# Kernel optimization log

Hardware: AMD Instinct MI355X
Metric: run time of the kernel (lower is better)

Reference implementation:

```python
import jax, jax.numpy as jnp
import numpy as np


def _gcn_conv(x, edge_index, edge_weight, W, b, n_nodes):
    # PyG GCNConv with normalize=True: add self-loops (weight 1), symmetric norm,
    # transform then aggregate: out[col] += norm * (x @ W)[row], plus bias.
    row = jnp.concatenate([edge_index[0], jnp.arange(n_nodes)])
    col = jnp.concatenate([edge_index[1], jnp.arange(n_nodes)])
    w = jnp.concatenate([edge_weight, jnp.ones((n_nodes,), x.dtype)])
    deg = jax.ops.segment_sum(w, col, num_segments=n_nodes)
    dinv = jnp.where(deg > 0, jax.lax.rsqrt(jnp.maximum(deg, 1e-12)), 0.0)
    norm = dinv[row] * w * dinv[col]            # [E+N]
    h = x @ W                                   # [N, out]
    msg = h[row] * norm[:, None]                # [E+N, out]
    out = jax.ops.segment_sum(msg, col, num_segments=n_nodes)
    return out + b


def setup_inputs() -> dict:
    key = jax.random.key(0)
    ks = jax.random.split(key, 6)
    N, E, F_IN, H, C = 50000, 800000, 512, 128, 40
    features = jax.random.normal(ks[0], (N, F_IN), jnp.float32)
    edge_index = jax.random.randint(ks[1], (2, E), 0, N, jnp.int64)
    edge_weight = jax.random.uniform(ks[2], (E,), jnp.float32)
    W1 = jax.random.normal(ks[3], (F_IN, H), jnp.float32) * 0.05
    b1 = jnp.zeros((H,), jnp.float32)
    W2 = jax.random.normal(ks[4], (H, C), jnp.float32) * 0.05
    b2 = jnp.zeros((C,), jnp.float32)
    return {"features": features, "edge_index": edge_index, "edge_weight": edge_weight,
            "W1": W1, "b1": b1, "W2": W2, "b2": b2}


def reference(features, edge_index, edge_weight, W1, b1, W2, b2):
    n_nodes = features.shape[0]
    x = _gcn_conv(features, edge_index, edge_weight, W1, b1, n_nodes)
    x = jax.nn.relu(x)
    # F.dropout(training=self.training): identity in eval mode
    x = _gcn_conv(x, edge_index, edge_weight, W2, b2, n_nodes)
    return jax.nn.log_softmax(x, axis=1)
```

## Files before the change

kernel.cpp:

```cpp
#include <hip/hip_runtime.h>
#include <math.h>

#define FIN  512
#define HDIM 128
#define CDIM 40
#define CPAD 48
#define H2P  40
#define CAP  64

typedef __attribute__((ext_vector_type(8))) short shortx8;
typedef __attribute__((ext_vector_type(4))) float f32x4;

__device__ inline unsigned short f2bf(float x) {
    unsigned u = __builtin_bit_cast(unsigned, x);
    unsigned r = u + 0x7fffu + ((u >> 16) & 1u);
    return (unsigned short)(r >> 16);
}
__device__ inline float bfu(unsigned short v) { return __builtin_bit_cast(float, (unsigned)v << 16); }
__device__ inline float bflo(unsigned u) { return __builtin_bit_cast(float, u << 16); }
__device__ inline float bfhi(unsigned u) { return __builtin_bit_cast(float, u & 0xffff0000u); }
__device__ inline float wdec(unsigned p) { return __builtin_bit_cast(float, (p & 0x7fffu) << 16); }

__global__ void k_fill(const int* __restrict__ row, const int* __restrict__ col,
                       const float* __restrict__ w,
                       unsigned long long* __restrict__ cursor,
                       unsigned* __restrict__ bkt, int E) {
    int e = blockIdx.x * blockDim.x + threadIdx.x;
    if (e >= E) return;
    const int c = col[e];
    const float we = w[e];
    const unsigned long long wfix = (unsigned long long)(we * 4294967296.0f);
    const unsigned long long old = atomicAdd(&cursor[c], (1ULL << 40) | wfix);
    const int p = (int)(old >> 40);
    const unsigned wb = (__builtin_bit_cast(unsigned, we) + 0x8000u) >> 16;
    if (p < CAP) bkt[(size_t)c * CAP + p] = ((unsigned)row[e] << 15) | (wb & 0x7fffu);
}

#define PREPB 280
__global__ void k_prep(const float* __restrict__ W1, const float* __restrict__ W2,
                       unsigned short* __restrict__ W1T, unsigned short* __restrict__ W2T,
                       const unsigned long long* __restrict__ cursor,
                       int* __restrict__ cnt, float* __restrict__ dinv, int n) {
    const int b = blockIdx.x;
    if (b < PREPB) {
        const int i = b * 256 + threadIdx.x;
        if (i < FIN * HDIM) {
            const int k = i >> 7, nn = i & 127;
            W1T[nn * FIN + k] = f2bf(W1[i]);
        } else {
            const int j = i - FIN * HDIM;
            const int nn = j >> 7, k = j & 127;
            W2T[j] = (nn < CDIM) ? f2bf(W2[k * CDIM + nn]) : (unsigned short)0;
        }
    } else {
        const int i = (b - PREPB) * 256 + threadIdx.x;
        if (i < n) {
            const unsigned long long p = cursor[i];
            cnt[i] = min((int)(p >> 40), CAP);
            const float wsum = (float)(p & ((1ULL << 40) - 1)) * 2.3283064365386963e-10f;
            dinv[i] = rsqrtf(1.0f + wsum);
        }
    }
}

#define G1_LDA 72
__global__ __launch_bounds__(256) void k_gemm1(const float* __restrict__ A,
                                               const unsigned short* __restrict__ W1T,
                                               const float* __restrict__ dinv,
                                               unsigned short* __restrict__ h1bf, int M) {
    __shared__ short As[128 * G1_LDA];
    __shared__ short Bs[128 * G1_LDA];
    const int tid  = threadIdx.x;
    const int wave = tid >> 6;
    const int lane = tid & 63;
    const int quad = lane >> 4;
    const int mr   = lane & 15;
    const int m0w  = (wave & 1) * 64;
    const int n0w  = (wave >> 1) * 64;
    const int m0b  = blockIdx.x * 128;

    const int srow = tid >> 1;
    const int spart = tid & 1;

    f32x4 acc[4][4];
#pragma unroll
    for (int i = 0; i < 4; i++)
#pragma unroll
        for (int j = 0; j < 4; j++) acc[i][j] = (f32x4)0.f;

    const int grow = m0b + srow;
    const bool arow_ok = grow < M;
    const float* ap = A + (size_t)grow * FIN + spart * 32;
    const unsigned short* bp = W1T + (size_t)srow * FIN + spart * 32;

    for (int k0 = 0; k0 < FIN; k0 += 64) {
#pragma unroll
        for (int i = 0; i < 4; i++) {
            float4 v0 = make_float4(0.f, 0.f, 0.f, 0.f), v1 = v0;
            if (arow_ok) {
                v0 = *(const float4*)(ap + k0 + i * 8);
                v1 = *(const float4*)(ap + k0 + i * 8 + 4);
            }
            shortx8 pk;
            pk[0] = (short)f2bf(v0.x); pk[1] = (short)f2bf(v0.y);
            pk[2] = (short)f2bf(v0.z); pk[3] = (short)f2bf(v0.w);
            pk[4] = (short)f2bf(v1.x); pk[5] = (short)f2bf(v1.y);
            pk[6] = (short)f2bf(v1.z); pk[7] = (short)f2bf(v1.w);
            *(shortx8*)&As[srow * G1_LDA + spart * 32 + i * 8] = pk;
        }
#pragma unroll
        for (int i = 0; i < 4; i++)
            *(shortx8*)&Bs[srow * G1_LDA + spart * 32 + i * 8] =
                *(const shortx8*)(bp + k0 + i * 8);
        __syncthreads();

#pragma unroll
        for (int kk = 0; kk < 2; kk++) {
            shortx8 af[4], bfr[4];
#pragma unroll
            for (int mt = 0; mt < 4; mt++)
                af[mt] = *(shortx8*)&As[(m0w + mt * 16 + mr) * G1_LDA + kk * 32 + quad * 8];
#pragma unroll
            for (int nt = 0; nt < 4; nt++)
                bfr[nt] = *(shortx8*)&Bs[(n0w + nt * 16 + mr) * G1_LDA + kk * 32 + quad * 8];
#pragma unroll
            for (int mt = 0; mt < 4; mt++)
#pragma unroll
                for (int nt = 0; nt < 4; nt++)
                    acc[mt][nt] = __builtin_amdgcn_mfma_f32_16x16x32_bf16(
                        af[mt], bfr[nt], acc[mt][nt], 0, 0, 0);
        }
        __syncthreads();
    }
#pragma unroll
    for (int mt = 0; mt < 4; mt++)
#pragma unroll
        for (int r = 0; r < 4; r++) {
            const int om = m0b + m0w + mt * 16 + quad * 4 + r;
            if (om < M) {
                const float dv = dinv[om];
#pragma unroll
                for (int nt = 0; nt < 4; nt++)
                    h1bf[(size_t)om * HDIM + n0w + nt * 16 + mr] = f2bf(dv * acc[mt][nt][r]);
            }
        }
}

__global__ __launch_bounds__(256) void k_gather1(
    const int* __restrict__ cnt_arr, const unsigned* __restrict__ bkt,
    const unsigned* __restrict__ h32,
    const float* __restrict__ dinv, const float* __restrict__ b1,
    unsigned* __restrict__ x1u, int n_nodes) {
    const int node = blockIdx.x * 4 + (threadIdx.x >> 6);
    const int lane = threadIdx.x & 63;
    if (node >= n_nodes) return;
    const int cnt = cnt_arr[node];
    const unsigned* base = bkt + (size_t)node * CAP;
    float a0 = 0.f, a1 = 0.f, c0 = 0.f, c1 = 0.f;
    int s = 0;
    for (; s + 8 <= cnt; s += 8) {
        const uint4 qa = *(const uint4*)(base + s);
        const uint4 qb = *(const uint4*)(base + s + 4);
        const unsigned u0 = h32[(size_t)(qa.x >> 15) * 64 + lane];
        const unsigned u1 = h32[(size_t)(qa.y >> 15) * 64 + lane];
        const unsigned u2 = h32[(size_t)(qa.z >> 15) * 64 + lane];
        const unsigned u3 = h32[(size_t)(qa.w >> 15) * 64 + lane];
        const unsigned u4 = h32[(size_t)(qb.x >> 15) * 64 + lane];
        const unsigned u5 = h32[(size_t)(qb.y >> 15) * 64 + lane];
        const unsigned u6 = h32[(size_t)(qb.z >> 15) * 64 + lane];
        const unsigned u7 = h32[(size_t)(qb.w >> 15) * 64 + lane];
        a0 += wdec(qa.x) * bflo(u0) + wdec(qa.y) * bflo(u1)
            + wdec(qa.z) * bflo(u2) + wdec(qa.w) * bflo(u3);
        a1 += wdec(qa.x) * bfhi(u0) + wdec(qa.y) * bfhi(u1)
            + wdec(qa.z) * bfhi(u2) + wdec(qa.w) * bfhi(u3);
        c0 += wdec(qb.x) * bflo(u4) + wdec(qb.y) * bflo(u5)
            + wdec(qb.z) * bflo(u6) + wdec(qb.w) * bflo(u7);
        c1 += wdec(qb.x) * bfhi(u4) + wdec(qb.y) * bfhi(u5)
            + wdec(qb.z) * bfhi(u6) + wdec(qb.w) * bfhi(u7);
    }
    for (; s + 4 <= cnt; s += 4) {
        const uint4 qa = *(const uint4*)(base + s);
        const unsigned u0 = h32[(size_t)(qa.x >> 15) * 64 + lane];
        const unsigned u1 = h32[(size_t)(qa.y >> 15) * 64 + lane];
        const unsigned u2 = h32[(size_t)(qa.z >> 15) * 64 + lane];
        const unsigned u3 = h32[(size_t)(qa.w >> 15) * 64 + lane];
        a0 += wdec(qa.x) * bflo(u0) + wdec(qa.y) * bflo(u1)
            + wdec(qa.z) * bflo(u2) + wdec(qa.w) * bflo(u3);
        a1 += wdec(qa.x) * bfhi(u0) + wdec(qa.y) * bfhi(u1)
            + wdec(qa.z) * bfhi(u2) + wdec(qa.w) * bfhi(u3);
    }
    for (; s < cnt; s++) {
        const unsigned p = base[s];
        const unsigned u = h32[(size_t)(p >> 15) * 64 + lane];
        a0 += wdec(p) * bflo(u);
        a1 += wdec(p) * bfhi(u);
    }
    a0 += c0; a1 += c1;
    const float dl = dinv[node];
    const unsigned us = h32[(size_t)node * 64 + lane];
    a0 = fmaxf(dl * (a0 + bflo(us)) + b1[lane * 2], 0.f);
    a1 = fmaxf(dl * (a1 + bfhi(us)) + b1[lane * 2 + 1], 0.f);
    x1u[(size_t)node * 64 + lane] = (unsigned)f2bf(a0) | ((unsigned)f2bf(a1) << 16);
}

#define G2_LDA 136
__global__ __launch_bounds__(256) void k_gemm2(const unsigned short* __restrict__ x1bf,
                                               const unsigned short* __restrict__ W2T,
                                               const float* __restrict__ dinv,
                                               unsigned short* __restrict__ h2bf, int M) {
    __shared__ short Xs[128 * G2_LDA];
    __shared__ short Ws[CPAD * G2_LDA];
    const int tid  = threadIdx.x;
    const int wave = tid >> 6;
    const int lane = tid & 63;
    const int quad = lane >> 4;
    const int mr   = lane & 15;
    const int m0b  = blockIdx.x * 128;

    {
        const int srow = tid >> 1, spart = tid & 1;
        const int grow = m0b + srow;
        if (grow < M) {
            const unsigned short* xp = x1bf + (size_t)grow * HDIM + spart * 64;
#pragma unroll
            for (int i = 0; i < 8; i++)
                *(shortx8*)&Xs[srow * G2_LDA + spart * 64 + i * 8] = *(const shortx8*)(xp + i * 8);
        } else {
#pragma unroll
            for (int i = 0; i < 8; i++)
                *(shortx8*)&Xs[srow * G2_LDA + spart * 64 + i * 8] = (shortx8)0;
        }
        for (int idx = tid; idx < CPAD * 16; idx += 256) {
            const int r = idx >> 4, j = idx & 15;
            *(shortx8*)&Ws[r * G2_LDA + j * 8] = *(const shortx8*)(W2T + r * HDIM + j * 8);
        }
    }
    __syncthreads();

    f32x4 acc[2][3];
#pragma unroll
    for (int i = 0; i < 2; i++)
#pragma unroll
        for (int j = 0; j < 3; j++) acc[i][j] = (f32x4)0.f;

    const int m0w = wave * 32;
#pragma unroll
    for (int kk = 0; kk < 4; kk++) {
        shortx8 af[2], bfr[3];
#pragma unroll
        for (int mt = 0; mt < 2; mt++)
            af[mt] = *(shortx8*)&Xs[(m0w + mt * 16 + mr) * G2_LDA + kk * 32 + quad * 8];
#pragma unroll
        for (int nt = 0; nt < 3; nt++)
            bfr[nt] = *(shortx8*)&Ws[(nt * 16 + mr) * G2_LDA + kk * 32 + quad * 8];
#pragma unroll
        for (int mt = 0; mt < 2; mt++)
#pragma unroll
            for (int nt = 0; nt < 3; nt++)
                acc[mt][nt] = __builtin_amdgcn_mfma_f32_16x16x32_bf16(
                    af[mt], bfr[nt], acc[mt][nt], 0, 0, 0);
    }
#pragma unroll
    for (int mt = 0; mt < 2; mt++)
#pragma unroll
        for (int r = 0; r < 4; r++) {
            const int om = m0b + m0w + mt * 16 + quad * 4 + r;
            if (om < M) {
                const float dv = dinv[om];
#pragma unroll
                for (int nt = 0; nt < 3; nt++) {
                    const int col = nt * 16 + mr;
                    if (col < CDIM)
                        h2bf[(size_t)om * H2P + col] = f2bf(dv * acc[mt][nt][r]);
                }
            }
        }
}

__global__ __launch_bounds__(256) void k_gather2(
    const int* __restrict__ cnt_arr, const unsigned* __restrict__ bkt,
    const unsigned short* __restrict__ h2bf,
    const float* __restrict__ dinv, const float* __restrict__ b2,
    float* __restrict__ out, int n_nodes) {
    const int node = blockIdx.x * 4 + (threadIdx.x >> 6);
    const int lane = threadIdx.x & 63;
    if (node >= n_nodes) return;
    const bool act = lane < CDIM;
    const int cnt = cnt_arr[node];
    const unsigned* base = bkt + (size_t)node * CAP;
    float acc = 0.f, accb = 0.f;
    int s = 0;
    for (; s + 4 <= cnt; s += 4) {
        const uint4 q = *(const uint4*)(base + s);
        if (act) {
            acc  += wdec(q.x) * bfu(h2bf[(size_t)(q.x >> 15) * H2P + lane])
                  + wdec(q.y) * bfu(h2bf[(size_t)(q.y >> 15) * H2P + lane]);
            accb += wdec(q.z) * bfu(h2bf[(size_t)(q.z >> 15) * H2P + lane])
                  + wdec(q.w) * bfu(h2bf[(size_t)(q.w >> 15) * H2P + lane]);
        }
    }
    for (; s < cnt; s++) {
        const unsigned p = base[s];
        if (act) acc += wdec(p) * bfu(h2bf[(size_t)(p >> 15) * H2P + lane]);
    }
    acc += accb;
    if (act) {
        const float dl = dinv[node];
        acc = dl * (acc + bfu(h2bf[(size_t)node * H2P + lane])) + b2[lane];
    }
    float m = act ? acc : -INFINITY;
#pragma unroll
    for (int off = 32; off; off >>= 1) m = fmaxf(m, __shfl_xor(m, off));
    float se = act ? expf(acc - m) : 0.f;
#pragma unroll
    for (int off = 32; off; off >>= 1) se += __shfl_xor(se, off);
    if (act) out[(size_t)node * CDIM + lane] = acc - m - logf(se);
}

extern "C" void kernel_launch(void* const* d_in, const int* in_sizes, int n_in,
                              void* d_out, int out_size, void* d_ws, size_t ws_size,
                              hipStream_t stream) {
    const float* features = (const float*)d_in[0];
    const int*   eidx     = (const int*)d_in[1];
    const float* ew       = (const float*)d_in[2];
    const float* W1       = (const float*)d_in[3];
    const float* b1       = (const float*)d_in[4];
    const float* W2       = (const float*)d_in[5];
    const float* b2       = (const float*)d_in[6];
    float* out = (float*)d_out;

    const int Nn = in_sizes[0] / FIN;
    const int E  = in_sizes[2];
    const int* row = eidx;
    const int* col = eidx + E;

    char* ws = (char*)d_ws;
    size_t off = 0;
    auto alloc = [&](size_t bytes) { void* p = ws + off; off += (bytes + 255) & ~(size_t)255; return p; };
    unsigned long long* cursor = (unsigned long long*)alloc((size_t)Nn * 8);
    int*      cnt          = (int*)     alloc((size_t)Nn * 4);
    float*    dinv         = (float*)   alloc((size_t)Nn * 4);
    unsigned* bkt          = (unsigned*)alloc((size_t)Nn * CAP * 4);
    unsigned short* W1T    = (unsigned short*)alloc((size_t)FIN * HDIM * 2);
    unsigned short* W2T    = (unsigned short*)alloc((size_t)CPAD * HDIM * 2);
    unsigned short* h1bf   = (unsigned short*)alloc((size_t)Nn * HDIM * 2);
    unsigned short* x1bf   = (unsigned short*)alloc((size_t)Nn * HDIM * 2);
    unsigned short* h2bf   = (unsigned short*)alloc(((size_t)Nn * H2P + 32) * 2);

    hipMemsetAsync(cursor, 0, (size_t)Nn * 8, stream);
    k_fill<<<(E + 255) / 256, 256, 0, stream>>>(row, col, ew, cursor, bkt, E);
    k_prep<<<PREPB + (Nn + 255) / 256, 256, 0, stream>>>(W1, W2, W1T, W2T,
                                                         cursor, cnt, dinv, Nn);
    k_gemm1<<<(Nn + 127) / 128, 256, 0, stream>>>(features, W1T, dinv, h1bf, Nn);
    k_gather1<<<(Nn + 3) / 4, 256, 0, stream>>>(cnt, bkt, (const unsigned*)h1bf,
                                                dinv, b1, (unsigned*)x1bf, Nn);
    k_gemm2<<<(Nn + 127) / 128, 256, 0, stream>>>(x1bf, W2T, dinv, h2bf, Nn);
    k_gather2<<<(Nn + 3) / 4, 256, 0, stream>>>(cnt, bkt, h2bf, dinv, b2, out, Nn);
}
```

Measured before the change: 310.4 us.

## Store layer-1 hidden features in fp8 and split layer-2 features into aligned arrays

```diff
diff --git a/kernel.cpp b/kernel.cpp
--- a/kernel.cpp
+++ b/kernel.cpp
@@ -5,11 +5,11 @@
 #define HDIM 128
 #define CDIM 40
 #define CPAD 48
-#define H2P  40
 #define CAP  64
 
 typedef __attribute__((ext_vector_type(8))) short shortx8;
 typedef __attribute__((ext_vector_type(4))) float f32x4;
+typedef __attribute__((ext_vector_type(2))) float floatx2;
 
 __device__ inline unsigned short f2bf(float x) {
     unsigned u = __builtin_bit_cast(unsigned, x);
@@ -20,6 +20,12 @@
 __device__ inline float bflo(unsigned u) { return __builtin_bit_cast(float, u << 16); }
 __device__ inline float bfhi(unsigned u) { return __builtin_bit_cast(float, u & 0xffff0000u); }
 __device__ inline float wdec(unsigned p) { return __builtin_bit_cast(float, (p & 0x7fffu) << 16); }
+__device__ inline unsigned char f2fp8(float x) {
+    return (unsigned char)(__builtin_amdgcn_cvt_pk_fp8_f32(x, x, 0, false) & 0xff);
+}
+__device__ inline floatx2 fp8x2_dec(unsigned short v) {
+    return __builtin_amdgcn_cvt_pk_f32_fp8((int)(unsigned)v, false);
+}
 
 __global__ void k_fill(const int* __restrict__ row, const int* __restrict__ col,
                        const float* __restrict__ w,
@@ -67,7 +73,7 @@
 __global__ __launch_bounds__(256) void k_gemm1(const float* __restrict__ A,
                                                const unsigned short* __restrict__ W1T,
                                                const float* __restrict__ dinv,
-                                               unsigned short* __restrict__ h1bf, int M) {
+                                               unsigned char* __restrict__ h1f8, int M) {
     __shared__ short As[128 * G1_LDA];
     __shared__ short Bs[128 * G1_LDA];
     const int tid  = threadIdx.x;
@@ -141,14 +147,14 @@
                 const float dv = dinv[om];
 #pragma unroll
                 for (int nt = 0; nt < 4; nt++)
-                    h1bf[(size_t)om * HDIM + n0w + nt * 16 + mr] = f2bf(dv * acc[mt][nt][r]);
+                    h1f8[(size_t)om * HDIM + n0w + nt * 16 + mr] = f2fp8(dv * acc[mt][nt][r]);
             }
         }
 }
 
 __global__ __launch_bounds__(256) void k_gather1(
     const int* __restrict__ cnt_arr, const unsigned* __restrict__ bkt,
-    const unsigned* __restrict__ h32,
+    const unsigned char* __restrict__ h1f8,
     const float* __restrict__ dinv, const float* __restrict__ b1,
     unsigned* __restrict__ x1u, int n_nodes) {
     const int node = blockIdx.x * 4 + (threadIdx.x >> 6);
@@ -156,50 +162,50 @@
     if (node >= n_nodes) return;
     const int cnt = cnt_arr[node];
     const unsigned* base = bkt + (size_t)node * CAP;
+    const int loff = lane * 2;
     float a0 = 0.f, a1 = 0.f, c0 = 0.f, c1 = 0.f;
     int s = 0;
     for (; s + 8 <= cnt; s += 8) {
         const uint4 qa = *(const uint4*)(base + s);
         const uint4 qb = *(const uint4*)(base + s + 4);
-        const unsigned u0 = h32[(size_t)(qa.x >> 15) * 64 + lane];
-        const unsigned u1 = h32[(size_t)(qa.y >> 15) * 64 + lane];
-        const unsigned u2 = h32[(size_t)(qa.z >> 15) * 64 + lane];
-        const unsigned u3 = h32[(size_t)(qa.w >> 15) * 64 + lane];
-        const unsigned u4 = h32[(size_t)(qb.x >> 15) * 64 + lane];
-        const unsigned u5 = h32[(size_t)(qb.y >> 15) * 64 + lane];
-        const unsigned u6 = h32[(size_t)(qb.z >> 15) * 64 + lane];
-        const unsigned u7 = h32[(size_t)(qb.w >> 15) * 64 + lane];
-        a0 += wdec(qa.x) * bflo(u0) + wdec(qa.y) * bflo(u1)
-            + wdec(qa.z) * bflo(u2) + wdec(qa.w) * bflo(u3);
-        a1 += wdec(qa.x) * bfhi(u0) + wdec(qa.y) * bfhi(u1)
-            + wdec(qa.z) * bfhi(u2) + wdec(qa.w) * bfhi(u3);
-        c0 += wdec(qb.x) * bflo(u4) + wdec(qb.y) * bflo(u5)
-            + wdec(qb.z) * bflo(u6) + wdec(qb.w) * bflo(u7);
-        c1 += wdec(qb.x) * bfhi(u4) + wdec(qb.y) * bfhi(u5)
-            + wdec(qb.z) * bfhi(u6) + wdec(qb.w) * bfhi(u7);
+        const unsigned short v0 = *(const unsigned short*)(h1f8 + (size_t)(qa.x >> 15) * HDIM + loff);
+        const unsigned short v1 = *(const unsigned short*)(h1f8 + (size_t)(qa.y >> 15) * HDIM + loff);
+        const unsigned short v2 = *(const unsigned short*)(h1f8 + (size_t)(qa.z >> 15) * HDIM + loff);
+        const unsigned short v3 = *(const unsigned short*)(h1f8 + (size_t)(qa.w >> 15) * HDIM + loff);
+        const unsigned short v4 = *(const unsigned short*)(h1f8 + (size_t)(qb.x >> 15) * HDIM + loff);
+        const unsigned short v5 = *(const unsigned short*)(h1f8 + (size_t)(qb.y >> 15) * HDIM + loff);
+        const unsigned short v6 = *(const unsigned short*)(h1f8 + (size_t)(qb.z >> 15) * HDIM + loff);
+        const unsigned short v7 = *(const unsigned short*)(h1f8 + (size_t)(qb.w >> 15) * HDIM + loff);
+        const floatx2 f0 = fp8x2_dec(v0), f1 = fp8x2_dec(v1), f2 = fp8x2_dec(v2), f3 = fp8x2_dec(v3);
+        const floatx2 f4 = fp8x2_dec(v4), f5 = fp8x2_dec(v5), f6 = fp8x2_dec(v6), f7 = fp8x2_dec(v7);
+        a0 += wdec(qa.x) * f0.x + wdec(qa.y) * f1.x + wdec(qa.z) * f2.x + wdec(qa.w) * f3.x;
+        a1 += wdec(qa.x) * f0.y + wdec(qa.y) * f1.y + wdec(qa.z) * f2.y + wdec(qa.w) * f3.y;
+        c0 += wdec(qb.x) * f4.x + wdec(qb.y) * f5.x + wdec(qb.z) * f6.x + wdec(qb.w) * f7.x;
+        c1 += wdec(qb.x) * f4.y + wdec(qb.y) * f5.y + wdec(qb.z) * f6.y + wdec(qb.w) * f7.y;
     }
     for (; s + 4 <= cnt; s += 4) {
         const uint4 qa = *(const uint4*)(base + s);
-        const unsigned u0 = h32[(size_t)(qa.x >> 15) * 64 + lane];
-        const unsigned u1 = h32[(size_t)(qa.y >> 15) * 64 + lane];
-        const unsigned u2 = h32[(size_t)(qa.z >> 15) * 64 + lane];
-        const unsigned u3 = h32[(size_t)(qa.w >> 15) * 64 + lane];
-        a0 += wdec(qa.x) * bflo(u0) + wdec(qa.y) * bflo(u1)
-            + wdec(qa.z) * bflo(u2) + wdec(qa.w) * bflo(u3);
-        a1 += wdec(qa.x) * bfhi(u0) + wdec(qa.y) * bfhi(u1)
-            + wdec(qa.z) * bfhi(u2) + wdec(qa.w) * bfhi(u3);
+        const unsigned short v0 = *(const unsigned short*)(h1f8 + (size_t)(qa.x >> 15) * HDIM + loff);
+        const unsigned short v1 = *(const unsigned short*)(h1f8 + (size_t)(qa.y >> 15) * HDIM + loff);
+        const unsigned short v2 = *(const unsigned short*)(h1f8 + (size_t)(qa.z >> 15) * HDIM + loff);
+        const unsigned short v3 = *(const unsigned short*)(h1f8 + (size_t)(qa.w >> 15) * HDIM + loff);
+        const floatx2 f0 = fp8x2_dec(v0), f1 = fp8x2_dec(v1), f2 = fp8x2_dec(v2), f3 = fp8x2_dec(v3);
+        a0 += wdec(qa.x) * f0.x + wdec(qa.y) * f1.x + wdec(qa.z) * f2.x + wdec(qa.w) * f3.x;
+        a1 += wdec(qa.x) * f0.y + wdec(qa.y) * f1.y + wdec(qa.z) * f2.y + wdec(qa.w) * f3.y;
     }
     for (; s < cnt; s++) {
         const unsigned p = base[s];
-        const unsigned u = h32[(size_t)(p >> 15) * 64 + lane];
-        a0 += wdec(p) * bflo(u);
-        a1 += wdec(p) * bfhi(u);
+        const unsigned short v = *(const unsigned short*)(h1f8 + (size_t)(p >> 15) * HDIM + loff);
+        const floatx2 f = fp8x2_dec(v);
+        a0 += wdec(p) * f.x;
+        a1 += wdec(p) * f.y;
     }
     a0 += c0; a1 += c1;
     const float dl = dinv[node];
-    const unsigned us = h32[(size_t)node * 64 + lane];
-    a0 = fmaxf(dl * (a0 + bflo(us)) + b1[lane * 2], 0.f);
-    a1 = fmaxf(dl * (a1 + bfhi(us)) + b1[lane * 2 + 1], 0.f);
+    const unsigned short vs = *(const unsigned short*)(h1f8 + (size_t)node * HDIM + loff);
+    const floatx2 fs = fp8x2_dec(vs);
+    a0 = fmaxf(dl * (a0 + fs.x) + b1[loff], 0.f);
+    a1 = fmaxf(dl * (a1 + fs.y) + b1[loff + 1], 0.f);
     x1u[(size_t)node * 64 + lane] = (unsigned)f2bf(a0) | ((unsigned)f2bf(a1) << 16);
 }
 
@@ -207,7 +213,8 @@
 __global__ __launch_bounds__(256) void k_gemm2(const unsigned short* __restrict__ x1bf,
                                                const unsigned short* __restrict__ W2T,
                                                const float* __restrict__ dinv,
-                                               unsigned short* __restrict__ h2bf, int M) {
+                                               unsigned short* __restrict__ h2a,
+                                               unsigned short* __restrict__ h2b, int M) {
     __shared__ short Xs[128 * G2_LDA];
     __shared__ short Ws[CPAD * G2_LDA];
     const int tid  = threadIdx.x;
@@ -268,18 +275,17 @@
             if (om < M) {
                 const float dv = dinv[om];
 #pragma unroll
-                for (int nt = 0; nt < 3; nt++) {
-                    const int col = nt * 16 + mr;
-                    if (col < CDIM)
-                        h2bf[(size_t)om * H2P + col] = f2bf(dv * acc[mt][nt][r]);
-                }
+                for (int nt = 0; nt < 2; nt++)
+                    h2a[(size_t)om * 32 + nt * 16 + mr] = f2bf(dv * acc[mt][nt][r]);
+                if (mr < 8)
+                    h2b[(size_t)om * 8 + mr] = f2bf(dv * acc[mt][2][r]);
             }
         }
 }
 
 __global__ __launch_bounds__(256) void k_gather2(
     const int* __restrict__ cnt_arr, const unsigned* __restrict__ bkt,
-    const unsigned short* __restrict__ h2bf,
+    const unsigned short* __restrict__ h2a, const unsigned short* __restrict__ h2b,
     const float* __restrict__ dinv, const float* __restrict__ b2,
     float* __restrict__ out, int n_nodes) {
     const int node = blockIdx.x * 4 + (threadIdx.x >> 6);
@@ -288,25 +294,27 @@
     const bool act = lane < CDIM;
     const int cnt = cnt_arr[node];
     const unsigned* base = bkt + (size_t)node * CAP;
+    const unsigned short* hb = (lane < 32) ? (h2a + lane) : (h2b + (lane & 31 & 7));
+    const int hstride = (lane < 32) ? 32 : 8;
     float acc = 0.f, accb = 0.f;
     int s = 0;
     for (; s + 4 <= cnt; s += 4) {
         const uint4 q = *(const uint4*)(base + s);
         if (act) {
-            acc  += wdec(q.x) * bfu(h2bf[(size_t)(q.x >> 15) * H2P + lane])
-                  + wdec(q.y) * bfu(h2bf[(size_t)(q.y >> 15) * H2P + lane]);
-            accb += wdec(q.z) * bfu(h2bf[(size_t)(q.z >> 15) * H2P + lane])
-                  + wdec(q.w) * bfu(h2bf[(size_t)(q.w >> 15) * H2P + lane]);
+            acc  += wdec(q.x) * bfu(hb[(size_t)(q.x >> 15) * hstride])
+                  + wdec(q.y) * bfu(hb[(size_t)(q.y >> 15) * hstride]);
+            accb += wdec(q.z) * bfu(hb[(size_t)(q.z >> 15) * hstride])
+                  + wdec(q.w) * bfu(hb[(size_t)(q.w >> 15) * hstride]);
         }
     }
     for (; s < cnt; s++) {
         const unsigned p = base[s];
-        if (act) acc += wdec(p) * bfu(h2bf[(size_t)(p >> 15) * H2P + lane]);
+        if (act) acc += wdec(p) * bfu(hb[(size_t)(p >> 15) * hstride]);
     }
     acc += accb;
     if (act) {
         const float dl = dinv[node];
-        acc = dl * (acc + bfu(h2bf[(size_t)node * H2P + lane])) + b2[lane];
+        acc = dl * (acc + bfu(hb[(size_t)node * hstride])) + b2[lane];
     }
     float m = act ? acc : -INFINITY;
 #pragma unroll
@@ -343,17 +351,18 @@
     unsigned* bkt          = (unsigned*)alloc((size_t)Nn * CAP * 4);
     unsigned short* W1T    = (unsigned short*)alloc((size_t)FIN * HDIM * 2);
     unsigned short* W2T    = (unsigned short*)alloc((size_t)CPAD * HDIM * 2);
-    unsigned short* h1bf   = (unsigned short*)alloc((size_t)Nn * HDIM * 2);
+    unsigned char*  h1f8   = (unsigned char*) alloc((size_t)Nn * HDIM);
     unsigned short* x1bf   = (unsigned short*)alloc((size_t)Nn * HDIM * 2);
-    unsigned short* h2bf   = (unsigned short*)alloc(((size_t)Nn * H2P + 32) * 2);
+    unsigned short* h2a    = (unsigned short*)alloc((size_t)Nn * 32 * 2);
+    unsigned short* h2b    = (unsigned short*)alloc((size_t)Nn * 8 * 2);
 
     hipMemsetAsync(cursor, 0, (size_t)Nn * 8, stream);
     k_fill<<<(E + 255) / 256, 256, 0, stream>>>(row, col, ew, cursor, bkt, E);
     k_prep<<<PREPB + (Nn + 255) / 256, 256, 0, stream>>>(W1, W2, W1T, W2T,
                                                          cursor, cnt, dinv, Nn);
-    k_gemm1<<<(Nn + 127) / 128, 256, 0, stream>>>(features, W1T, dinv, h1bf, Nn);
-    k_gather1<<<(Nn + 3) / 4, 256, 0, stream>>>(cnt, bkt, (const unsigned*)h1bf,
-                                                dinv, b1, (unsigned*)x1bf, Nn);
-    k_gemm2<<<(Nn + 127) / 128, 256, 0, stream>>>(x1bf, W2T, dinv, h2bf, Nn);
-    k_gather2<<<(Nn + 3) / 4, 256, 0, stream>>>(cnt, bkt, h2bf, dinv, b2, out, Nn);
-}
+    k_gemm1<<<(Nn + 127) / 128, 256, 0, stream>>>(features, W1T, dinv, h1f8, Nn);
+    k_gather1<<<(Nn + 3) / 4, 256, 0, stream>>>(cnt, bkt, h1f8, dinv, b1,
+                                                (unsigned*)x1bf, Nn);
+    k_gemm2<<<(Nn + 127) / 128, 256, 0, stream>>>(x1bf, W2T, dinv, h2a, h2b, Nn);
+    k_gather2<<<(Nn + 3) / 4, 256, 0, stream>>>(cnt, bkt, h2a, h2b, dinv, b2, out, Nn);
+}
```

Measured after the change: 302.3 us. -2.6%, faster.
